# Performance work log

Measured on AMD Instinct MI355X. Metric: run time of the kernel, lower is better.

## Reference

```python
import jax, jax.numpy as jnp
import numpy as np
from jax import lax

SEQ, IN, H, NC, L = 2048, 1024, 1024, 512, 3


def _lstm_layer(x_seq, W_ih, W_hh, b_ih, b_hh):
    # x_seq: [T, in] -> hs: [T, H]. PyTorch gate order: i, f, g, o.
    Hd = W_hh.shape[1]
    # Precompute input contribution for all timesteps (one big GEMM).
    gx = x_seq @ W_ih.T + (b_ih + b_hh)  # [T, 4H]

    def step(carry, gx_t):
        h, c = carry
        gates = gx_t + h @ W_hh.T  # [4H]
        i, f, g, o = jnp.split(gates, 4)
        i = jax.nn.sigmoid(i)
        f = jax.nn.sigmoid(f)
        g = jnp.tanh(g)
        o = jax.nn.sigmoid(o)
        c = f * c + i * g
        h = o * jnp.tanh(c)
        return (h, c), h

    h0 = jnp.zeros((Hd,), x_seq.dtype)
    c0 = jnp.zeros((Hd,), x_seq.dtype)
    _, hs = lax.scan(step, (h0, c0), gx)
    return hs


def setup_inputs() -> dict:
    key = jax.random.key(0)
    ks = jax.random.split(key, 16)
    s = 1.0 / np.sqrt(H)  # PyTorch LSTM init scale
    d = {"x": jax.random.normal(ks[0], (SEQ, IN), jnp.float32)}
    i = 1
    for l in range(L):
        in_dim = IN if l == 0 else H
        d[f"W_ih_{l}"] = jax.random.normal(ks[i], (4 * H, in_dim), jnp.float32) * s; i += 1
        d[f"W_hh_{l}"] = jax.random.normal(ks[i], (4 * H, H), jnp.float32) * s; i += 1
        d[f"b_ih_{l}"] = jax.random.normal(ks[i], (4 * H,), jnp.float32) * s; i += 1
        d[f"b_hh_{l}"] = jax.random.normal(ks[i], (4 * H,), jnp.float32) * s; i += 1
    d["fc_w"] = jax.random.normal(ks[13], (NC, H), jnp.float32) * s
    d["fc_b"] = jax.random.normal(ks[14], (NC,), jnp.float32) * s
    return d


def reference(x, W_ih_0, W_hh_0, b_ih_0, b_hh_0,
              W_ih_1, W_hh_1, b_ih_1, b_hh_1,
              W_ih_2, W_hh_2, b_ih_2, b_hh_2,
              fc_w, fc_b):
    h = _lstm_layer(x, W_ih_0, W_hh_0, b_ih_0, b_hh_0)
    h = _lstm_layer(h, W_ih_1, W_hh_1, b_ih_1, b_hh_1)
    h = _lstm_layer(h, W_ih_2, W_hh_2, b_ih_2, b_hh_2)
    return h @ fc_w.T + fc_b  # [SEQ, NC]
```

## Files before the change

### kernel.cpp

```cpp
#include <hip/hip_runtime.h>

#define HDIM  1024
#define FOURH 4096
#define TSEQ  2048
#define NCLS  512

#define SCANB  64
#define GEMMB  32
#define U16    16
#define DRING  128
#define GXRING 128
#define CHUNK  64
#define NCHUNK 32

#define CNT0 0
#define CNT1 64
#define CD0  128
#define CD1  192
#define SP1  256
#define SP2  320
#define SYNC_BYTES 2048
#define HDR_BYTES 32768

typedef float v2f __attribute__((ext_vector_type(2)));

union SharedU {
    struct { float h[HDIM]; float gate[4][U16]; } scan;
    struct { float As[16][72]; float Bs[16][132]; } gemm;
};

__device__ __forceinline__ unsigned long long ald(const unsigned long long* p) {
    return __hip_atomic_load(p, __ATOMIC_RELAXED, __HIP_MEMORY_SCOPE_AGENT);
}
__device__ __forceinline__ void ast(unsigned long long* p, unsigned long long v) {
    __hip_atomic_store(p, v, __ATOMIC_RELAXED, __HIP_MEMORY_SCOPE_AGENT);
}
__device__ __forceinline__ unsigned ald32(const unsigned* p) {
    return __hip_atomic_load(p, __ATOMIC_RELAXED, __HIP_MEMORY_SCOPE_AGENT);
}
__device__ __forceinline__ void ast32(unsigned* p, unsigned v) {
    __hip_atomic_store(p, v, __ATOMIC_RELAXED, __HIP_MEMORY_SCOPE_AGENT);
}

__device__ __forceinline__ float fsig(float x)  { return 1.f / (1.f + __expf(-x)); }
__device__ __forceinline__ float ftanh(float x) { return 1.f - 2.f / (1.f + __expf(2.f * x)); }

__global__ __launch_bounds__(256) void gemm_bias_kernel(
    const float* __restrict__ A, const float* __restrict__ B,
    const float* __restrict__ bias1, const float* __restrict__ bias2,
    float* __restrict__ C, int M, int N, int K)
{
    __shared__ float As[16][68];
    __shared__ float Bs[16][68];

    const int tid = threadIdx.x;
    const int tx = tid & 15;
    const int ty = tid >> 4;
    const int n0 = blockIdx.x * 64;
    const int m0 = blockIdx.y * 64;
    const int r  = tid >> 2;
    const int kq = tid & 3;

    float acc[4][4];
#pragma unroll
    for (int i = 0; i < 4; ++i)
#pragma unroll
        for (int j = 0; j < 4; ++j) acc[i][j] = 0.f;

    for (int k0 = 0; k0 < K; k0 += 16) {
        float4 va = *(const float4*)&A[(size_t)(m0 + r) * K + k0 + 4 * kq];
        float4 vb = *(const float4*)&B[(size_t)(n0 + r) * K + k0 + 4 * kq];
        As[4 * kq + 0][r] = va.x; As[4 * kq + 1][r] = va.y;
        As[4 * kq + 2][r] = va.z; As[4 * kq + 3][r] = va.w;
        Bs[4 * kq + 0][r] = vb.x; Bs[4 * kq + 1][r] = vb.y;
        Bs[4 * kq + 2][r] = vb.z; Bs[4 * kq + 3][r] = vb.w;
        __syncthreads();
#pragma unroll
        for (int kk = 0; kk < 16; ++kk) {
            float4 a = *(const float4*)&As[kk][4 * ty];
            float4 b = *(const float4*)&Bs[kk][4 * tx];
            acc[0][0] = fmaf(a.x, b.x, acc[0][0]);
            acc[0][1] = fmaf(a.x, b.y, acc[0][1]);
            acc[0][2] = fmaf(a.x, b.z, acc[0][2]);
            acc[0][3] = fmaf(a.x, b.w, acc[0][3]);
            acc[1][0] = fmaf(a.y, b.x, acc[1][0]);
            acc[1][1] = fmaf(a.y, b.y, acc[1][1]);
            acc[1][2] = fmaf(a.y, b.z, acc[1][2]);
            acc[1][3] = fmaf(a.y, b.w, acc[1][3]);
            acc[2][0] = fmaf(a.z, b.x, acc[2][0]);
            acc[2][1] = fmaf(a.z, b.y, acc[2][1]);
            acc[2][2] = fmaf(a.z, b.z, acc[2][2]);
            acc[2][3] = fmaf(a.z, b.w, acc[2][3]);
            acc[3][0] = fmaf(a.w, b.x, acc[3][0]);
            acc[3][1] = fmaf(a.w, b.y, acc[3][1]);
            acc[3][2] = fmaf(a.w, b.z, acc[3][2]);
            acc[3][3] = fmaf(a.w, b.w, acc[3][3]);
        }
        __syncthreads();
    }

    float4 bv = *(const float4*)&bias1[n0 + 4 * tx];
    if (bias2) {
        float4 b2 = *(const float4*)&bias2[n0 + 4 * tx];
        bv.x += b2.x; bv.y += b2.y; bv.z += b2.z; bv.w += b2.w;
    }
#pragma unroll
    for (int i = 0; i < 4; ++i) {
        const int row = m0 + 4 * ty + i;
        float4 o;
        o.x = acc[i][0] + bv.x;
        o.y = acc[i][1] + bv.y;
        o.z = acc[i][2] + bv.z;
        o.w = acc[i][3] + bv.w;
        *(float4*)&C[(size_t)row * N + n0 + 4 * tx] = o;
    }
}

#define LOAD_GXS(T) do { if (lane < 8) {                                      \
    gxs = __uint_as_float(ald32((const unsigned*)gxb +                        \
        (size_t)((T) & gxmask) * FOURH + (size_t)(lane >> 1) * HDIM           \
        + u0 + 2 * w + (lane & 1))); }                                        \
    gxrow = __shfl(gxs, lane & 7, 64); } while (0)

__device__ void scan_role(int bi,
    const float* __restrict__ Whh,
    const unsigned long long* __restrict__ gxb, unsigned gxmask,
    unsigned long long* __restrict__ ring,
    const unsigned* cdSrc,
    const unsigned* cdBp,
    unsigned* sp,
    float* __restrict__ h2,
    SharedU* sm, unsigned* hcnt)
{
    const int tid  = threadIdx.x;
    const int w    = tid >> 6;
    const int lane = tid & 63;
    const int uu   = lane & 1;
    const int u0   = bi * U16;

    v2f wv[8][8];
#pragma unroll
    for (int rg = 0; rg < 8; ++rg) {
        const float* Wr = Whh +
            (size_t)((rg >> 1) * HDIM + u0 + 2 * w + (rg & 1)) * HDIM;
#pragma unroll
        for (int j = 0; j < 4; ++j) {
            const float4 q = *(const float4*)(Wr + 256 * j + 4 * lane);
            v2f qa = {q.x, q.y}, qb = {q.z, q.w};
            wv[rg][2 * j]     = qa;
            wv[rg][2 * j + 1] = qb;
        }
    }
    { float2 z = {0.f, 0.f}; *(float2*)(sm->scan.h + 2 * tid) = z; }
    if (tid == 0) *hcnt = 0u;
    float cst = 0.f;
    float gxs = 0.f;
    float gxrow = 0.f;
    unsigned cdc = 0u, bpc = 0u;
    __syncthreads();

    for (int t = 0; t < TSEQ; ++t) {
        if (cdBp && t >= DRING && w == 7 && lane == 0) {
            const unsigned need = (unsigned)((t - DRING) >> 6) + 1u;
            while (bpc < need) {
                bpc = ald32(cdBp);
                if (bpc < need) __builtin_amdgcn_s_sleep(4);
            }
        }
        if ((t & (CHUNK - 1)) == 0) {
            if (cdSrc && lane == 0) {
                const unsigned need = (unsigned)(t >> 6) + 1u;
                while (cdc < need) {
                    cdc = ald32(cdSrc);
                    if (cdc < need) __builtin_amdgcn_s_sleep(4);
                }
            }
            LOAD_GXS(t);
        }

        v2f acc2[8];
#pragma unroll
        for (int rg = 0; rg < 8; ++rg) { v2f z = {0.f, 0.f}; acc2[rg] = z; }
#pragma unroll
        for (int j = 0; j < 4; ++j) {
            const float4 hq = *(const float4*)(sm->scan.h + 256 * j + 4 * lane);
            const v2f hA = {hq.x, hq.y};
            const v2f hB = {hq.z, hq.w};
#pragma unroll
            for (int rg = 0; rg < 8; ++rg) {
                acc2[rg] = __builtin_elementwise_fma(wv[rg][2 * j],     hA, acc2[rg]);
                acc2[rg] = __builtin_elementwise_fma(wv[rg][2 * j + 1], hB, acc2[rg]);
            }
        }
        float a[8];
#pragma unroll
        for (int rg = 0; rg < 8; ++rg) a[rg] = acc2[rg].x + acc2[rg].y;

#pragma unroll
        for (int off = 1; off <= 4; off <<= 1)
#pragma unroll
            for (int rg = 0; rg < 8; ++rg)
                a[rg] += __shfl_xor(a[rg], off, 64);
        const int l7 = lane & 7;
        const float s0 = (l7 & 1) ? a[1] : a[0];
        const float s1 = (l7 & 1) ? a[3] : a[2];
        const float s2 = (l7 & 1) ? a[5] : a[4];
        const float s3 = (l7 & 1) ? a[7] : a[6];
        const float t0 = (l7 & 2) ? s1 : s0;
        const float t1 = (l7 & 2) ? s3 : s2;
        float x = (l7 & 4) ? t1 : t0;
        x += __shfl_xor(x, 8, 64);
        x += __shfl_xor(x, 16, 64);
        x += __shfl_xor(x, 32, 64);
        x += gxrow;

        float gsum[4];
#pragma unroll
        for (int g = 0; g < 4; ++g)
            gsum[g] = __shfl(x, 2 * g + uu, 64);
        {
            const float si = fsig(gsum[0]), sf = fsig(gsum[1]);
            const float tg = ftanh(gsum[2]), so = fsig(gsum[3]);
            cst = sf * cst + si * tg;
            const float hval = so * ftanh(cst);
            if (lane < 2) {
                sm->scan.gate[0][2 * w + lane] = hval;
                if (h2) h2[(size_t)t * HDIM + u0 + 2 * w + lane] = hval;
            }
        }
        asm volatile("s_waitcnt lgkmcnt(0)" ::: "memory");
        if (lane == 0)
            __hip_atomic_fetch_add(hcnt, 1u, __ATOMIC_RELAXED,
                                   __HIP_MEMORY_SCOPE_WORKGROUP);

        const unsigned tag = (unsigned)(t + 1);
        if (w == 7) {
            const unsigned needC = 8u * (unsigned)(t + 1);
            while (__hip_atomic_load(hcnt, __ATOMIC_RELAXED,
                                     __HIP_MEMORY_SCOPE_WORKGROUP) < needC) {}
            asm volatile("s_waitcnt lgkmcnt(0)" ::: "memory");
            __builtin_amdgcn_sched_barrier(0);
            if (lane < U16) {
                const float h = sm->scan.gate[0][lane];
                ast(ring + (size_t)(t & (DRING - 1)) * HDIM + u0 + lane,
                    ((unsigned long long)tag << 32) |
                    (unsigned long long)__float_as_uint(h));
            }
            if (sp && bi == 0 && lane == 0) ast32(sp, (unsigned)t);
        }
        if (((t + 1) & (CHUNK - 1)) != 0 && t + 1 < TSEQ) LOAD_GXS(t + 1);

        if (t + 1 < TSEQ) {
            const unsigned long long* hb = ring + (size_t)(t & (DRING - 1)) * HDIM;
            unsigned long long v0 = 0, v1 = 0;
            bool got0 = false, got1 = false;
            while (!(got0 && got1)) {
                if (!got0) {
                    const unsigned long long y = ald(hb + 2 * tid);
                    if ((unsigned)(y >> 32) == tag) { v0 = y; got0 = true; }
                }
                if (!got1) {
                    const unsigned long long y = ald(hb + 2 * tid + 1);
                    if ((unsigned)(y >> 32) == tag) { v1 = y; got1 = true; }
                }
                if (!(got0 && got1)) __builtin_amdgcn_s_sleep(1);
            }
            __syncthreads();
            sm->scan.h[2 * tid]     = __uint_as_float((unsigned)v0);
            sm->scan.h[2 * tid + 1] = __uint_as_float((unsigned)v1);
            __syncthreads();
        }
    }
}

__device__ void gemm_role(int tix,
    const unsigned long long* __restrict__ ringS,
    const float* __restrict__ Wih,
    const float* __restrict__ bih, const float* __restrict__ bhh,
    float* __restrict__ gxr,
    unsigned* cnt, unsigned* cd, const unsigned* spC,
    SharedU* sm)
{
    const int tid = threadIdx.x;
    const int tx = tid & 31, ty = tid >> 5;
    const int n0 = tix * 128;
    const int tt = tid >> 3, ke = tid & 7;
    const int cB = tid >> 2, kq = tid & 3;

    float4 bv;
    {
        const float4 b1 = *(const float4*)(bih + n0 + 4 * tx);
        const float4 b2 = *(const float4*)(bhh + n0 + 4 * tx);
        bv.x = b1.x + b2.x; bv.y = b1.y + b2.y;
        bv.z = b1.z + b2.z; bv.w = b1.w + b2.w;
    }
    unsigned long long* gxr64 = (unsigned long long*)gxr;

    for (int q = 0; q < NCHUNK; ++q) {
        if (q >= GXRING / CHUNK && tid == 0) {
            const unsigned need = (unsigned)((q - GXRING / CHUNK + 1) * CHUNK + 2);
            while (ald32(spC) < need) __builtin_amdgcn_s_sleep(8);
        }
        __syncthreads();

        float acc[4][4];
#pragma unroll
        for (int i = 0; i < 4; ++i)
#pragma unroll
            for (int j = 0; j < 4; ++j) acc[i][j] = 0.f;

        for (int k0 = 0; k0 < HDIM; k0 += 16) {
            {
                const int trow = q * CHUNK + tt;
                const unsigned expt = (unsigned)(trow + 1);
                const unsigned long long* srcp =
                    ringS + (size_t)(trow & (DRING - 1)) * HDIM + k0 + 2 * ke;
#pragma unroll
                for (int e = 0; e < 2; ++e) {
                    unsigned long long x;
                    while ((unsigned)((x = ald(srcp + e)) >> 32) != expt)
                        __builtin_amdgcn_s_sleep(1);
                    sm->gemm.As[2 * ke + e][tt] = __uint_as_float((unsigned)x);
                }
            }
            {
                const float4 vb = *(const float4*)(Wih + (size_t)(n0 + cB) * HDIM + k0 + 4 * kq);
                sm->gemm.Bs[4 * kq + 0][cB] = vb.x;
                sm->gemm.Bs[4 * kq + 1][cB] = vb.y;
                sm->gemm.Bs[4 * kq + 2][cB] = vb.z;
                sm->gemm.Bs[4 * kq + 3][cB] = vb.w;
            }
            __syncthreads();
#pragma unroll
            for (int kk = 0; kk < 16; ++kk) {
                const float4 a = *(const float4*)&sm->gemm.As[kk][4 * ty];
                const float4 b = *(const float4*)&sm->gemm.Bs[kk][4 * tx];
                acc[0][0] = fmaf(a.x, b.x, acc[0][0]);
                acc[0][1] = fmaf(a.x, b.y, acc[0][1]);
                acc[0][2] = fmaf(a.x, b.z, acc[0][2]);
                acc[0][3] = fmaf(a.x, b.w, acc[0][3]);
                acc[1][0] = fmaf(a.y, b.x, acc[1][0]);
                acc[1][1] = fmaf(a.y, b.y, acc[1][1]);
                acc[1][2] = fmaf(a.y, b.z, acc[1][2]);
                acc[1][3] = fmaf(a.y, b.w, acc[1][3]);
                acc[2][0] = fmaf(a.z, b.x, acc[2][0]);
                acc[2][1] = fmaf(a.z, b.y, acc[2][1]);
                acc[2][2] = fmaf(a.z, b.z, acc[2][2]);
                acc[2][3] = fmaf(a.z, b.w, acc[2][3]);
                acc[3][0] = fmaf(a.w, b.x, acc[3][0]);
                acc[3][1] = fmaf(a.w, b.y, acc[3][1]);
                acc[3][2] = fmaf(a.w, b.z, acc[3][2]);
                acc[3][3] = fmaf(a.w, b.w, acc[3][3]);
            }
            __syncthreads();
        }

#pragma unroll
        for (int i = 0; i < 4; ++i) {
            const int trow = q * CHUNK + 4 * ty + i;
            const float o0 = acc[i][0] + bv.x;
            const float o1 = acc[i][1] + bv.y;
            const float o2 = acc[i][2] + bv.z;
            const float o3 = acc[i][3] + bv.w;
            const size_t base =
                ((size_t)(trow & (GXRING - 1)) * FOURH + n0 + 4 * tx) / 2;
            ast(gxr64 + base,
                ((unsigned long long)__float_as_uint(o1) << 32) | __float_as_uint(o0));
            ast(gxr64 + base + 1,
                ((unsigned long long)__float_as_uint(o3) << 32) | __float_as_uint(o2));
        }
        asm volatile("s_waitcnt vmcnt(0)" ::: "memory");
        __syncthreads();
        if (tid == 0) {
            const unsigned old = __hip_atomic_fetch_add(cnt + q, 1u,
                                     __ATOMIC_RELAXED, __HIP_MEMORY_SCOPE_AGENT);
            if (old + 1u == (unsigned)GEMMB) ast32(cd, (unsigned)(q + 1));
        }
    }
}

__global__ __launch_bounds__(512, 2) void fused_scan(
    const float* __restrict__ gx0,
    const float* __restrict__ Whh0, const float* __restrict__ Whh1,
    const float* __restrict__ Whh2,
    const float* __restrict__ Wih1, const float* __restrict__ Wih2,
    const float* __restrict__ bih1, const float* __restrict__ bhh1,
    const float* __restrict__ bih2, const float* __restrict__ bhh2,
    unsigned long long* ring0, unsigned long long* ring1, unsigned long long* ring2,
    float* gxr1, float* gxr2,
    float* h2out, unsigned* syncw)
{
    __shared__ SharedU sm;
    __shared__ unsigned hcnt;
    const int lb = blockIdx.x;
    if (lb < 3 * SCANB) {
        const int layer = lb >> 6;
        const int bi    = lb & 63;
        if (layer == 0)
            scan_role(bi, Whh0, (const unsigned long long*)gx0, 2047u, ring0,
                      nullptr, syncw + CD0, nullptr, nullptr, &sm, &hcnt);
        else if (layer == 1)
            scan_role(bi, Whh1, (const unsigned long long*)gxr1, GXRING - 1u, ring1,
                      syncw + CD0, syncw + CD1, syncw + SP1, nullptr, &sm, &hcnt);
        else
            scan_role(bi, Whh2, (const unsigned long long*)gxr2, GXRING - 1u, ring2,
                      syncw + CD1, nullptr, syncw + SP2, h2out, &sm, &hcnt);
    } else {
        const int gb  = lb - 3 * SCANB;
        const int gl  = gb >> 5;
        const int tix = gb & 31;
        if (gl == 0)
            gemm_role(tix, ring0, Wih1, bih1, bhh1, gxr1,
                      syncw + CNT0, syncw + CD0, syncw + SP1, &sm);
        else
            gemm_role(tix, ring1, Wih2, bih2, bhh2, gxr2,
                      syncw + CNT1, syncw + CD1, syncw + SP2, &sm);
    }
}

extern "C" void kernel_launch(void* const* d_in, const int* in_sizes, int n_in,
                              void* d_out, int out_size, void* d_ws, size_t ws_size,
                              hipStream_t stream)
{
    (void)in_sizes; (void)n_in; (void)out_size; (void)ws_size;

    const float* x = (const float*)d_in[0];
    const float* W_ih[3] = {(const float*)d_in[1], (const float*)d_in[5], (const float*)d_in[9]};
    const float* W_hh[3] = {(const float*)d_in[2], (const float*)d_in[6], (const float*)d_in[10]};
    const float* b_ih[3] = {(const float*)d_in[3], (const float*)d_in[7], (const float*)d_in[11]};
    const float* b_hh[3] = {(const float*)d_in[4], (const float*)d_in[8], (const float*)d_in[12]};
    const float* fc_w = (const float*)d_in[13];
    const float* fc_b = (const float*)d_in[14];
    float* out = (float*)d_out;

    unsigned* syncw = (unsigned*)d_ws;
    float* gx = (float*)((char*)d_ws + HDR_BYTES);
    float* A  = gx + (size_t)TSEQ * FOURH;
    unsigned long long* ring0 = (unsigned long long*)(A + (size_t)TSEQ * HDIM);
    unsigned long long* ring1 = ring0 + (size_t)DRING * HDIM;
    unsigned long long* ring2 = ring1 + (size_t)DRING * HDIM;
    float* gxr1 = (float*)(ring2 + (size_t)DRING * HDIM);
    float* gxr2 = gxr1 + (size_t)GXRING * FOURH;

    hipMemsetAsync(syncw, 0, SYNC_BYTES, stream);

    {
        dim3 g(FOURH / 64, TSEQ / 64);
        gemm_bias_kernel<<<g, 256, 0, stream>>>(x, W_ih[0], b_ih[0], b_hh[0],
                                                gx, TSEQ, FOURH, HDIM);
    }

    {
        const float* gx0_c = gx;
        float* h2 = A;
        void* args[] = {
            (void*)&gx0_c,
            (void*)&W_hh[0], (void*)&W_hh[1], (void*)&W_hh[2],
            (void*)&W_ih[1], (void*)&W_ih[2],
            (void*)&b_ih[1], (void*)&b_hh[1],
            (void*)&b_ih[2], (void*)&b_hh[2],
            (void*)&ring0, (void*)&ring1, (void*)&ring2,
            (void*)&gxr1, (void*)&gxr2,
            (void*)&h2, (void*)&syncw
        };
        hipLaunchCooperativeKernel((void*)fused_scan,
                                   dim3(3 * SCANB + 2 * GEMMB), dim3(512),
                                   args, 0, stream);
    }

    {
        dim3 g(NCLS / 64, TSEQ / 64);
        gemm_bias_kernel<<<g, 256, 0, stream>>>(A, fc_w, fc_b, nullptr,
                                                out, TSEQ, NCLS, HDIM);
    }
}
```

Before: 7.727 ms.

## Poll h ring with 16-byte loads and gate GEMM chunks on scan progress

The scan blocks' spin-wait on the next hidden-state slot now issues one 16-byte global load with cache-bypass bits in place of two separate 64-bit atomic loads, checking both tags from one read. The GEMM blocks also wait, through a new progress counter published by layer 0, until the producing scan layer has finished a whole chunk before starting it. This is meant to cut polling traffic and keep GEMM blocks from spinning per element on slots that are not ready. The extra wait may add latency for the GEMM role, and the 16-byte load is not formally atomic, which relies on each tag/value pair being written as one 8-byte store.

Measured after the change: 7.663 ms. About the same (-0.8%).

```diff
diff --git a/kernel.cpp b/kernel.cpp
--- a/kernel.cpp
+++ b/kernel.cpp
@@ -19,10 +19,12 @@
 #define CD1  192
 #define SP1  256
 #define SP2  320
+#define SP0  384
 #define SYNC_BYTES 2048
 #define HDR_BYTES 32768
 
 typedef float v2f __attribute__((ext_vector_type(2)));
+typedef unsigned int u32x4 __attribute__((ext_vector_type(4)));
 
 union SharedU {
     struct { float h[HDIM]; float gate[4][U16]; } scan;
@@ -40,6 +42,13 @@
 }
 __device__ __forceinline__ void ast32(unsigned* p, unsigned v) {
     __hip_atomic_store(p, v, __ATOMIC_RELAXED, __HIP_MEMORY_SCOPE_AGENT);
+}
+__device__ __forceinline__ u32x4 ald16B(const unsigned long long* p) {
+    u32x4 y;
+    asm volatile("global_load_dwordx4 %0, %1, off sc0 sc1\n\t"
+                 "s_waitcnt vmcnt(0)"
+                 : "=v"(y) : "v"(p) : "memory");
+    return y;
 }
 
 __device__ __forceinline__ float fsig(float x)  { return 1.f / (1.f + __expf(-x)); }
@@ -252,22 +261,18 @@
 
         if (t + 1 < TSEQ) {
             const unsigned long long* hb = ring + (size_t)(t & (DRING - 1)) * HDIM;
-            unsigned long long v0 = 0, v1 = 0;
+            const unsigned long long* addr = hb + 2 * tid;
+            unsigned h0 = 0, h1 = 0;
             bool got0 = false, got1 = false;
             while (!(got0 && got1)) {
-                if (!got0) {
-                    const unsigned long long y = ald(hb + 2 * tid);
-                    if ((unsigned)(y >> 32) == tag) { v0 = y; got0 = true; }
-                }
-                if (!got1) {
-                    const unsigned long long y = ald(hb + 2 * tid + 1);
-                    if ((unsigned)(y >> 32) == tag) { v1 = y; got1 = true; }
-                }
+                const u32x4 y = ald16B(addr);
+                if (!got0 && y.y == tag) { h0 = y.x; got0 = true; }
+                if (!got1 && y.w == tag) { h1 = y.z; got1 = true; }
                 if (!(got0 && got1)) __builtin_amdgcn_s_sleep(1);
             }
             __syncthreads();
-            sm->scan.h[2 * tid]     = __uint_as_float((unsigned)v0);
-            sm->scan.h[2 * tid + 1] = __uint_as_float((unsigned)v1);
+            sm->scan.h[2 * tid]     = __uint_as_float(h0);
+            sm->scan.h[2 * tid + 1] = __uint_as_float(h1);
             __syncthreads();
         }
     }
@@ -275,6 +280,7 @@
 
 __device__ void gemm_role(int tix,
     const unsigned long long* __restrict__ ringS,
+    const unsigned* __restrict__ spA,
     const float* __restrict__ Wih,
     const float* __restrict__ bih, const float* __restrict__ bhh,
     float* __restrict__ gxr,
@@ -300,6 +306,10 @@
         if (q >= GXRING / CHUNK && tid == 0) {
             const unsigned need = (unsigned)((q - GXRING / CHUNK + 1) * CHUNK + 2);
             while (ald32(spC) < need) __builtin_amdgcn_s_sleep(8);
+        }
+        if (tid == 0) {
+            const unsigned needA = (unsigned)(q * CHUNK + CHUNK - 1);
+            while (ald32(spA) < needA) __builtin_amdgcn_s_sleep(16);
         }
         __syncthreads();
 
@@ -398,7 +408,7 @@
         const int bi    = lb & 63;
         if (layer == 0)
             scan_role(bi, Whh0, (const unsigned long long*)gx0, 2047u, ring0,
-                      nullptr, syncw + CD0, nullptr, nullptr, &sm, &hcnt);
+                      nullptr, syncw + CD0, syncw + SP0, nullptr, &sm, &hcnt);
         else if (layer == 1)
             scan_role(bi, Whh1, (const unsigned long long*)gxr1, GXRING - 1u, ring1,
                       syncw + CD0, syncw + CD1, syncw + SP1, nullptr, &sm, &hcnt);
@@ -410,10 +420,10 @@
         const int gl  = gb >> 5;
         const int tix = gb & 31;
         if (gl == 0)
-            gemm_role(tix, ring0, Wih1, bih1, bhh1, gxr1,
+            gemm_role(tix, ring0, syncw + SP0, Wih1, bih1, bhh1, gxr1,
                       syncw + CNT0, syncw + CD0, syncw + SP1, &sm);
         else
-            gemm_role(tix, ring1, Wih2, bih2, bhh2, gxr2,
+            gemm_role(tix, ring1, syncw + SP1, Wih2, bih2, bhh2, gxr2,
                       syncw + CNT1, syncw + CD1, syncw + SP2, &sm);
     }
 }
```
